# Performance work log

Hardware: AMD Instinct MI355X
Metric: run time of the kernel (lower is better)

## Reference

```python
import jax, jax.numpy as jnp
import numpy as np
import math

T = 4096
HID = 2048
H = 16
D = 128
RD = 64            # rotary_dim = head_dim * partial_rotary_factor (0.5)
THETA = 10000.0
EPS = 1e-6
GROUPS = 8
LAYER_IDX = 2
N_LAYERS = 32


def build_slope_tensor(num_heads):
    def get_slopes_power_of_2(n):
        start = 2 ** (-(2 ** (-(math.log2(n) - 3))))
        ratio = start
        return [start * ratio ** i for i in range(n)]
    if math.log2(num_heads).is_integer():
        return get_slopes_power_of_2(num_heads)
    closest = 2 ** math.floor(math.log2(num_heads))
    return (get_slopes_power_of_2(closest)
            + build_slope_tensor(2 * closest)[0::2][: num_heads - closest])


def compute_slope():
    base = np.array(build_slope_tensor(H), dtype=np.float32)
    return jnp.asarray(-base * (1 - (LAYER_IDX - 1) / (N_LAYERS - 1) + 1e-5), dtype=jnp.float32)


def setup_inputs() -> dict:
    key = jax.random.key(0)
    ks = jax.random.split(key, 8)
    s = 0.02
    return {
        "positions": jnp.arange(T, dtype=jnp.int32),
        "hidden_states": jax.random.normal(ks[0], (T, HID), dtype=jnp.float32),
        "recurrent_state": jnp.zeros((1, H, D, D), dtype=jnp.float32),
        "w_qkv": jax.random.normal(ks[1], (HID, 3 * H * D), dtype=jnp.float32) * s,
        "w_g": jax.random.normal(ks[2], (HID, H * D), dtype=jnp.float32) * s,
        "w_dense": jax.random.normal(ks[3], (H * D, HID), dtype=jnp.float32) * s,
        "q_norm_w": jnp.ones((D,), dtype=jnp.float32),
        "k_norm_w": jnp.ones((D,), dtype=jnp.float32),
        "g_norm_w": jnp.ones((H * D,), dtype=jnp.float32),
    }


def _rms(x, w):
    var = jnp.mean(jnp.square(x), axis=-1, keepdims=True)
    return x * jax.lax.rsqrt(var + EPS) * w


def _rope(x, positions):
    # partial neox-style rotary on first RD dims of each head
    inv_freq = 1.0 / (THETA ** (jnp.arange(0, RD, 2, dtype=jnp.float32) / RD))
    freqs = positions.astype(jnp.float32)[:, None] * inv_freq   # [T, RD/2]
    cos = jnp.cos(freqs)[:, None, :]                            # [T, 1, RD/2]
    sin = jnp.sin(freqs)[:, None, :]
    x1 = x[..., : RD // 2]
    x2 = x[..., RD // 2 : RD]
    x_pass = x[..., RD:]
    return jnp.concatenate([x1 * cos - x2 * sin, x2 * cos + x1 * sin, x_pass], axis=-1)


def reference(positions, hidden_states, recurrent_state,
              w_qkv, w_g, w_dense, q_norm_w, k_norm_w, g_norm_w):
    t = hidden_states.shape[0]
    qkv = (hidden_states @ w_qkv).reshape(t, 3, H, D)
    q, k, v = qkv[:, 0], qkv[:, 1], qkv[:, 2]
    q = _rms(q, q_norm_w)
    k = _rms(k, k_norm_w)
    q = _rope(q, positions)
    k = _rope(k, positions)

    slope = compute_slope()                    # [H], negative
    decay = jnp.exp(slope)                     # per-head per-step decay
    scale = D ** -0.5
    q = (q * scale).astype(jnp.float32)
    k = k.astype(jnp.float32)
    v = v.astype(jnp.float32)

    def step(S, qkv_t):
        q_t, k_t, v_t = qkv_t                  # each [H, D]
        S = S * decay[:, None, None] + k_t[:, :, None] * v_t[:, None, :]
        o_t = jnp.einsum('hk,hkv->hv', q_t, S)
        return S, o_t

    S0 = recurrent_state[0].astype(jnp.float32)   # [H, K, V]
    S_final, o = jax.lax.scan(step, S0, (q, k, v))
    attn = o.reshape(t, H * D)

    gate = jax.nn.sigmoid(hidden_states @ w_g)
    # GroupRMSNorm: normalize per group of size (H*D)/GROUPS, scale by full weight
    g = attn.reshape(t, GROUPS, (H * D) // GROUPS)
    var = jnp.mean(jnp.square(g), axis=-1, keepdims=True)
    g = (g * jax.lax.rsqrt(var + EPS)).reshape(t, H * D) * g_norm_w

    out = (g * gate) @ w_dense
    return out, S_final[None]
```

## Files before the change

kernel.cpp:

```cpp
#include <hip/hip_runtime.h>
#include <hip/hip_bf16.h>

using bf16x8 = __attribute__((ext_vector_type(8))) __bf16;
using f32x4  = __attribute__((ext_vector_type(4))) float;

constexpr int T_SEQ = 4096;
constexpr int HID_C = 2048;
constexpr int NH    = 16;
constexpr int QKV_N = 6144;

__device__ __forceinline__ float head_slope(int h) {
    return -exp2f(-0.5f * (float)(h + 1)) * 0.967751935483871f;
}

__device__ __forceinline__ ushort f2bfu(float f) {
    __hip_bfloat16 h = __float2bfloat16(f);
    return *(ushort*)&h;
}
__device__ __forceinline__ float bfu2f(ushort u) {
    union { unsigned int i; float f; } x; x.i = ((unsigned int)u) << 16; return x.f;
}

__device__ __forceinline__ void async16(const ushort* g, ushort* l) {
    __builtin_amdgcn_global_load_lds((const __attribute__((address_space(1))) void*)g,
                                     (__attribute__((address_space(3))) void*)l, 16, 0, 0);
}

template<int N> __device__ __forceinline__ void waitcnt_vm() {
    if constexpr (N == 0)      asm volatile("s_waitcnt vmcnt(0)" ::: "memory");
    else if constexpr (N == 2) asm volatile("s_waitcnt vmcnt(2)" ::: "memory");
    else if constexpr (N == 4) asm volatile("s_waitcnt vmcnt(4)" ::: "memory");
    else if constexpr (N == 6) asm volatile("s_waitcnt vmcnt(6)" ::: "memory");
}

__global__ __launch_bounds__(256) void cvt_bf16(const float* __restrict__ src,
                                                ushort* __restrict__ dst, int n) {
    int i = (blockIdx.x * 256 + threadIdx.x) * 8;
    if (i >= n) return;
    float4 a = *(const float4*)(src + i);
    float4 b = *(const float4*)(src + i + 4);
    ushort4 ua = {f2bfu(a.x), f2bfu(a.y), f2bfu(a.z), f2bfu(a.w)};
    ushort4 ub = {f2bfu(b.x), f2bfu(b.y), f2bfu(b.z), f2bfu(b.w)};
    *(ushort4*)(dst + i) = ua;
    *(ushort4*)(dst + i + 4) = ub;
}

__global__ __launch_bounds__(256) void transpose_cvt(const float* __restrict__ src,
                                                     ushort* __restrict__ dst,
                                                     int R, int C) {
    __shared__ ushort tile[64][68];
    int t = threadIdx.x;
    int tr = blockIdx.y * 64, tc = blockIdx.x * 64;
    int r0 = t >> 4;
    int c4 = (t & 15) << 2;
#pragma unroll
    for (int p = 0; p < 4; ++p) {
        int row = r0 + p * 16;
        float4 v = *(const float4*)&src[(size_t)(tr + row) * C + tc + c4];
        tile[row][c4 + 0] = f2bfu(v.x);
        tile[row][c4 + 1] = f2bfu(v.y);
        tile[row][c4 + 2] = f2bfu(v.z);
        tile[row][c4 + 3] = f2bfu(v.w);
    }
    __syncthreads();
#pragma unroll
    for (int p = 0; p < 4; ++p) {
        int orow = r0 + p * 16;
        ushort4 u;
        u.x = tile[c4 + 0][orow];
        u.y = tile[c4 + 1][orow];
        u.z = tile[c4 + 2][orow];
        u.w = tile[c4 + 3][orow];
        *(ushort4*)&dst[(size_t)(tc + orow) * R + tr + c4] = u;
    }
}

template<int MI, int BN>
__device__ __forceinline__ void gemm8_core(const ushort* __restrict__ Ag,
                                           const ushort* __restrict__ Bg,
                                           int K, int bm, int bn,
                                           ushort* sh, f32x4 (&acc)[MI][4]) {
    constexpr int WM = 16 / MI;
    constexpr int WN = 8 / WM;
    constexpr int MP = MI / 4;
    constexpr int SB = BN / 128;

    const int tid  = threadIdx.x;
    const int lane = tid & 63;
    const int wave = tid >> 6;
    const int lane15 = lane & 15, quad = lane >> 4;
    const int wm = wave / WN, wn = wave % WN;
    const int swz = lane15 & 7;

    ushort* const ldsA0 = sh;
    ushort* const ldsA1 = sh + 16384;
    ushort* const ldsB0 = sh + 32768;
    ushort* const ldsB1 = sh + 32768 + BN * 64;

    const int srow = lane >> 3;
    const int scol = ((lane & 7) ^ srow) << 3;
    const ushort* gA = Ag + (size_t)(bm + srow) * K + scol;
    const ushort* gB = Bg + (size_t)(bn + srow) * K + scol;
    const int ro  = wave * 16;
    const int roB = wave * 8 * SB;
    const int NT = K >> 6;

#define ST_A(L, h, k0) do { \
    _Pragma("unroll") for (int q = 0; q < 2; ++q) \
        async16(gA + (size_t)((h) * 128 + ro + q * 8) * K + (k0), (L) + ((h) * 128 + ro + q * 8) * 64); } while (0)
#define ST_B(L, h, k0) do { \
    _Pragma("unroll") for (int q = 0; q < SB; ++q) \
        async16(gB + (size_t)((h) * (BN / 2) + roB + q * 8) * K + (k0), (L) + ((h) * (BN / 2) + roB + q * 8) * 64); } while (0)
#define RD_A(L, p) do { \
    _Pragma("unroll") for (int m2 = 0; m2 < MP; ++m2) \
    _Pragma("unroll") for (int ks = 0; ks < 2; ++ks) \
        afr[m2][ks] = *(const bf16x8*)&(L)[(wm * (MI * 16) + ((p) * MP + m2) * 16 + lane15) * 64 + (((ks * 4 + quad) ^ swz) << 3)]; } while (0)
#define RD_B(L) do { \
    _Pragma("unroll") for (int j = 0; j < 4; ++j) \
    _Pragma("unroll") for (int ks = 0; ks < 2; ++ks) \
        bfr[j][ks] = *(const bf16x8*)&(L)[(wn * 64 + j * 16 + lane15) * 64 + (((ks * 4 + quad) ^ swz) << 3)]; } while (0)
#define MFMA_PH(p) do { \
    asm volatile("s_barrier" ::: "memory"); \
    asm volatile("s_waitcnt lgkmcnt(0)" ::: "memory"); \
    __builtin_amdgcn_s_setprio(1); \
    _Pragma("unroll") for (int m2 = 0; m2 < MP; ++m2) \
    _Pragma("unroll") for (int j = 0; j < 4; ++j) \
    _Pragma("unroll") for (int ks = 0; ks < 2; ++ks) \
        acc[(p) * MP + m2][j] = __builtin_amdgcn_mfma_f32_16x16x32_bf16(afr[m2][ks], bfr[j][ks], acc[(p) * MP + m2][j], 0, 0, 0); \
    __builtin_amdgcn_s_setprio(0); } while (0)
#define KTILE(LAc, LBc, LAn, LBn, t) do { \
    const int k0 = (t) << 6; \
    bf16x8 bfr[4][2]; \
    bf16x8 afr[MP][2]; \
    RD_B(LBc); RD_A(LAc, 0); \
    if ((t) + 1 < NT) ST_A(LAn, 0, k0 + 64); \
    MFMA_PH(0); \
    asm volatile("s_barrier" ::: "memory"); \
    RD_A(LAc, 1); \
    if ((t) + 1 < NT) ST_A(LAn, 1, k0 + 64); \
    MFMA_PH(1); \
    asm volatile("s_barrier" ::: "memory"); \
    RD_A(LAc, 2); \
    if ((t) + 2 < NT) ST_B(LBc, 0, k0 + 128); \
    MFMA_PH(2); \
    asm volatile("s_barrier" ::: "memory"); \
    RD_A(LAc, 3); \
    if ((t) + 2 < NT) ST_B(LBc, 1, k0 + 128); \
    MFMA_PH(3); \
    if ((t) + 2 < NT) { waitcnt_vm<2 * SB>(); } \
    else              { waitcnt_vm<0>(); } \
    asm volatile("s_barrier" ::: "memory"); } while (0)

    ST_A(ldsA0, 0, 0); ST_A(ldsA0, 1, 0);
    ST_B(ldsB0, 0, 0); ST_B(ldsB0, 1, 0);
    ST_B(ldsB1, 0, 64); ST_B(ldsB1, 1, 64);
    waitcnt_vm<2 * SB>();
    asm volatile("s_barrier" ::: "memory");

    for (int t = 0; t < NT; t += 2) {
        KTILE(ldsA0, ldsB0, ldsA1, ldsB1, t);
        KTILE(ldsA1, ldsB1, ldsA0, ldsB0, t + 1);
    }
#undef ST_A
#undef ST_B
#undef RD_A
#undef RD_B
#undef MFMA_PH
#undef KTILE
}

__global__ __launch_bounds__(512, 2) void gemm_fused(const ushort* __restrict__ A,
                                                     const ushort* __restrict__ Bcat,
                                                     ushort* __restrict__ qkv,
                                                     ushort* __restrict__ gate, int K) {
    __shared__ ushort sh[65536];
    int bid = blockIdx.x;
    int x = bid & 7, w = bid >> 3;
    int rm = x >> 2, rn = x & 3;
    int wm_i = w >> 3, wn_i = w & 7;
    int bm = (rm * 8 + wm_i) * 256;
    int bn = (rn * 8 + wn_i) * 256;
    f32x4 acc[8][4] = {};
    gemm8_core<8, 256>(A, Bcat, K, bm, bn, sh, acc);

    int lane = threadIdx.x & 63, wave = threadIdx.x >> 6;
    int lane15 = lane & 15, quad = lane >> 4;
    int wm = wave >> 2, wn = wave & 3;
    bool isg = bn >= QKV_N;
    ushort* outp = isg ? gate : qkv;
    int ncol = isg ? HID_C : QKV_N;
    int cb = (isg ? bn - QKV_N : bn) + wn * 64;
    int rb = bm + wm * 128;
#pragma unroll
    for (int i = 0; i < 8; ++i)
#pragma unroll
        for (int j = 0; j < 4; ++j) {
            int col = cb + j * 16 + lane15;
#pragma unroll
            for (int r = 0; r < 4; ++r) {
                float v = acc[i][j][r];
                if (isg) v = 1.0f / (1.0f + __expf(-v));
                outp[(size_t)(rb + i * 16 + quad * 4 + r) * ncol + col] = f2bfu(v);
            }
        }
}

__global__ __launch_bounds__(512, 2) void gemm_dense(const ushort* __restrict__ A,
                                                     const ushort* __restrict__ Bt,
                                                     float* __restrict__ Cout, int N, int K) {
    __shared__ ushort sh[49152];
    int bid = blockIdx.x;
    int x = bid & 7, w = bid >> 3;
    int rm = x >> 1, rn = x & 1;
    int wm_i = w >> 3, wn_i = w & 7;
    int bm = (rm * 4 + wm_i) * 256;
    int bn = (rn * 8 + wn_i) * 128;
    f32x4 acc[4][4] = {};
    gemm8_core<4, 128>(A, Bt, K, bm, bn, sh, acc);

    int lane = threadIdx.x & 63, wave = threadIdx.x >> 6;
    int lane15 = lane & 15, quad = lane >> 4;
    int wm = wave >> 1, wn = wave & 1;
    int cb = bn + wn * 64;
    int rb = bm + wm * 64;
#pragma unroll
    for (int i = 0; i < 4; ++i)
#pragma unroll
        for (int j = 0; j < 4; ++j) {
            int col = cb + j * 16 + lane15;
#pragma unroll
            for (int r = 0; r < 4; ++r)
                Cout[(size_t)(rb + i * 16 + quad * 4 + r) * N + col] = acc[i][j][r];
        }
}

__global__ __launch_bounds__(256) void rope_tab(const int* __restrict__ positions,
                                                float2* __restrict__ tab) {
    int i = blockIdx.x * 256 + threadIdx.x;
    int t = i >> 5, fi = i & 31;
    float inv = expf((float)fi * -0.2878231366f);
    float freq = (float)positions[t] * inv;
    float sn, cs;
    sincosf(freq, &sn, &cs);
    tab[i] = make_float2(cs, sn);
}

__global__ __launch_bounds__(256) void qk_rope_T(ushort* __restrict__ qkv,
                                                 const float2* __restrict__ tab,
                                                 const float* __restrict__ qw,
                                                 const float* __restrict__ kw,
                                                 ushort* __restrict__ kT,
                                                 ushort* __restrict__ vT) {
    __shared__ ushort tile[64][132];
    int bt = blockIdx.x;
    int kind = blockIdx.y >> 4, h = blockIdx.y & 15;
    int tid = threadIdx.x;
    int row = tid >> 2, c = tid & 3, d0 = c * 32;
    int t = bt * 64 + row;
    ushort* base = qkv + (size_t)t * QKV_N + kind * 2048 + h * 128 + d0;
    bf16x8 pk[4];
#pragma unroll
    for (int p = 0; p < 4; ++p) pk[p] = *(const bf16x8*)(base + p * 8);
    if (kind < 2) {
        float x[32];
        float ss = 0.f;
#pragma unroll
        for (int p = 0; p < 4; ++p)
#pragma unroll
            for (int i = 0; i < 8; ++i) {
                x[p * 8 + i] = (float)pk[p][i];
                ss += x[p * 8 + i] * x[p * 8 + i];
            }
        ss += __shfl_xor(ss, 1);
        ss += __shfl_xor(ss, 2);
        float rr = rsqrtf(ss * (1.0f / 128.0f) + 1e-6f);
        const float* w = (kind == 0) ? qw : kw;
#pragma unroll
        for (int i = 0; i < 32; ++i) x[i] *= rr * w[d0 + i];
#pragma unroll
        for (int i = 0; i < 32; ++i) {
            float p = __shfl_xor(x[i], 1);
            if (c < 2) {
                float2 rt = tab[t * 32 + i];
                x[i] = (c == 0) ? (x[i] * rt.x - p * rt.y) : (x[i] * rt.x + p * rt.y);
            }
        }
        float sc = (kind == 0) ? 0.08838834764831845f : 1.0f;
#pragma unroll
        for (int p = 0; p < 4; ++p)
#pragma unroll
            for (int i = 0; i < 8; ++i) pk[p][i] = (__bf16)(x[p * 8 + i] * sc);
#pragma unroll
        for (int p = 0; p < 4; ++p) *(bf16x8*)(base + p * 8) = pk[p];
    }
    if (kind >= 1) {
#pragma unroll
        for (int p = 0; p < 4; ++p) {
            ushort4* s = (ushort4*)&pk[p];
            *(ushort4*)&tile[row][d0 + p * 8]     = s[0];
            *(ushort4*)&tile[row][d0 + p * 8 + 4] = s[1];
        }
        __syncthreads();
        ushort* outT = ((kind == 1) ? kT : vT) + (size_t)(h * 128) * T_SEQ + bt * 64;
        int d = tid >> 1, half = tid & 1;
#pragma unroll
        for (int tt = 0; tt < 8; ++tt) {
            int tl = half * 32 + tt * 4;
            ushort4 u;
            u.x = tile[tl + 0][d];
            u.y = tile[tl + 1][d];
            u.z = tile[tl + 2][d];
            u.w = tile[tl + 3][d];
            *(ushort4*)&outT[(size_t)d * T_SEQ + tl] = u;
        }
    }
}

__global__ __launch_bounds__(256) void chunk_partial(const ushort* __restrict__ kT,
                                                     const ushort* __restrict__ vT,
                                                     float* __restrict__ PT) {
    int c = blockIdx.x, h = blockIdx.y;
    float slope = head_slope(h);
    float lam_inv = __expf(-slope);
    int tid = threadIdx.x, lane = tid & 63, wave = tid >> 6;
    int lane15 = lane & 15, quad = lane >> 4;
    int wv = (wave & 1) * 64, wd = (wave >> 1) * 64;
    const ushort* vbase = vT + (size_t)h * 128 * T_SEQ + c * 128;
    const ushort* kbase = kT + (size_t)h * 128 * T_SEQ + c * 128;
    f32x4 acc[4][4] = {};
#pragma unroll
    for (int j0 = 0; j0 < 128; j0 += 32) {
        float w8[8];
        w8[0] = __expf(slope * (float)(127 - (j0 + quad * 8)));
#pragma unroll
        for (int kk = 1; kk < 8; ++kk) w8[kk] = w8[kk - 1] * lam_inv;
        bf16x8 afr[4], bfr[4];
#pragma unroll
        for (int i = 0; i < 4; ++i) {
            bf16x8 v = *(const bf16x8*)&vbase[(size_t)(wv + i * 16 + lane15) * T_SEQ + j0 + quad * 8];
#pragma unroll
            for (int kk = 0; kk < 8; ++kk) afr[i][kk] = (__bf16)((float)v[kk] * w8[kk]);
        }
#pragma unroll
        for (int j = 0; j < 4; ++j)
            bfr[j] = *(const bf16x8*)&kbase[(size_t)(wd + j * 16 + lane15) * T_SEQ + j0 + quad * 8];
#pragma unroll
        for (int i = 0; i < 4; ++i)
#pragma unroll
            for (int j = 0; j < 4; ++j)
                acc[i][j] = __builtin_amdgcn_mfma_f32_16x16x32_bf16(afr[i], bfr[j], acc[i][j], 0, 0, 0);
    }
    float* out = PT + ((size_t)c * 16 + h) * 16384;
#pragma unroll
    for (int i = 0; i < 4; ++i)
#pragma unroll
        for (int j = 0; j < 4; ++j)
#pragma unroll
            for (int r = 0; r < 4; ++r)
                out[(size_t)(wv + i * 16 + quad * 4 + r) * 128 + wd + j * 16 + lane15] = acc[i][j][r];
}

__global__ __launch_bounds__(128) void scan_states(const float* __restrict__ PT,
                                                   const float* __restrict__ S0,
                                                   ushort* __restrict__ Spb,
                                                   float* __restrict__ Sfin) {
    int hv = blockIdx.x;
    int d = threadIdx.x;
    int h = hv >> 7, v = hv & 127;
    float lamC = __expf(head_slope(h) * 128.0f);
    float s = S0[(size_t)h * 16384 + d * 128 + v];
#pragma unroll
    for (int c = 0; c < 32; ++c) {
        size_t idx = ((size_t)c * 2048 + hv) * 128 + d;
        Spb[idx] = f2bfu(s);
        s = s * lamC + PT[idx];
    }
    Sfin[(size_t)h * 16384 + d * 128 + v] = s;
}

__global__ __launch_bounds__(256) void chunk_out(const ushort* __restrict__ qkv,
                                                 const ushort* __restrict__ vT,
                                                 const ushort* __restrict__ Spb,
                                                 ushort* __restrict__ o) {
    int c = blockIdx.x, h = blockIdx.y;
    float slope = head_slope(h);
    __shared__ ushort Ps[128 * 136];
    int tid = threadIdx.x, lane = tid & 63, wave = tid >> 6;
    int lane15 = lane & 15, quad = lane >> 4;
    int t0 = c * 128;
    int tt0 = wave, tt1 = 7 - wave;
    const ushort* qbase = qkv + (size_t)t0 * QKV_N + h * 128;
    const ushort* kbase = qbase + 2048;

    bf16x8 qf0[4], qf1[4];
#pragma unroll
    for (int ds = 0; ds < 4; ++ds) {
        qf0[ds] = *(const bf16x8*)&qbase[(size_t)(tt0 * 16 + lane15) * QKV_N + ds * 32 + quad * 8];
        qf1[ds] = *(const bf16x8*)&qbase[(size_t)(tt1 * 16 + lane15) * QKV_N + ds * 32 + quad * 8];
    }
    f32x4 s0a[4] = {};
    f32x4 s1a[8] = {};
#pragma unroll
    for (int st = 0; st < 8; ++st) {
        if (st <= tt1) {
            bf16x8 kf[4];
#pragma unroll
            for (int ds = 0; ds < 4; ++ds)
                kf[ds] = *(const bf16x8*)&kbase[(size_t)(st * 16 + lane15) * QKV_N + ds * 32 + quad * 8];
#pragma unroll
            for (int ds = 0; ds < 4; ++ds)
                s1a[st] = __builtin_amdgcn_mfma_f32_16x16x32_bf16(qf1[ds], kf[ds], s1a[st], 0, 0, 0);
            if (st <= tt0) {
#pragma unroll
                for (int ds = 0; ds < 4; ++ds)
                    s0a[st] = __builtin_amdgcn_mfma_f32_16x16x32_bf16(qf0[ds], kf[ds], s0a[st], 0, 0, 0);
            }
        }
    }
    int stmax0 = tt0 + ((tt0 & 1) ? 0 : 1);
    int stmax1 = tt1 + ((tt1 & 1) ? 0 : 1);
#pragma unroll
    for (int st = 0; st < 8; ++st) {
        if (st <= stmax1) {
#pragma unroll
            for (int r = 0; r < 4; ++r) {
                int t = tt1 * 16 + quad * 4 + r;
                int s = st * 16 + lane15;
                float val = 0.f;
                if (st <= tt1) val = (s <= t) ? s1a[st][r] * __expf(slope * (float)(t - s)) : 0.f;
                Ps[t * 136 + s] = f2bfu(val);
            }
        }
    }
#pragma unroll
    for (int st = 0; st < 5; ++st) {
        if (st <= stmax0) {
#pragma unroll
            for (int r = 0; r < 4; ++r) {
                int t = tt0 * 16 + quad * 4 + r;
                int s = st * 16 + lane15;
                float val = 0.f;
                if (st <= tt0) val = (s <= t) ? s0a[st][r] * __expf(slope * (float)(t - s)) : 0.f;
                Ps[t * 136 + s] = f2bfu(val);
            }
        }
    }
    __syncthreads();
    f32x4 oa0[8] = {};
    f32x4 oa1[8] = {};
    float lam0 = __expf(slope * (float)(tt0 * 16 + lane15 + 1));
    float lam1 = __expf(slope * (float)(tt1 * 16 + lane15 + 1));
    bf16x8 qs0[4], qs1[4];
#pragma unroll
    for (int ds = 0; ds < 4; ++ds)
#pragma unroll
        for (int kk = 0; kk < 8; ++kk) {
            qs0[ds][kk] = (__bf16)((float)qf0[ds][kk] * lam0);
            qs1[ds][kk] = (__bf16)((float)qf1[ds][kk] * lam1);
        }
    const ushort* spb = Spb + ((size_t)c * 2048 + h * 128) * 128;
#pragma unroll
    for (int vt = 0; vt < 8; ++vt)
#pragma unroll
        for (int ds = 0; ds < 4; ++ds) {
            bf16x8 bfrag = *(const bf16x8*)&spb[(vt * 16 + lane15) * 128 + ds * 32 + quad * 8];
            oa0[vt] = __builtin_amdgcn_mfma_f32_16x16x32_bf16(qs0[ds], bfrag, oa0[vt], 0, 0, 0);
            oa1[vt] = __builtin_amdgcn_mfma_f32_16x16x32_bf16(qs1[ds], bfrag, oa1[vt], 0, 0, 0);
        }
    const ushort* vbase = vT + (size_t)h * 128 * T_SEQ + t0;
    int ns0 = (tt0 + 2) >> 1, ns1 = (tt1 + 2) >> 1;
#pragma unroll
    for (int s32 = 0; s32 < 4; ++s32) {
        if (s32 < ns1) {
            bf16x8 af = *(const bf16x8*)&Ps[(tt1 * 16 + lane15) * 136 + s32 * 32 + quad * 8];
#pragma unroll
            for (int vt = 0; vt < 8; ++vt) {
                bf16x8 bfrag = *(const bf16x8*)&vbase[(size_t)(vt * 16 + lane15) * T_SEQ + s32 * 32 + quad * 8];
                oa1[vt] = __builtin_amdgcn_mfma_f32_16x16x32_bf16(af, bfrag, oa1[vt], 0, 0, 0);
            }
        }
    }
#pragma unroll
    for (int s32 = 0; s32 < 2; ++s32) {
        if (s32 < ns0) {
            bf16x8 af = *(const bf16x8*)&Ps[(tt0 * 16 + lane15) * 136 + s32 * 32 + quad * 8];
#pragma unroll
            for (int vt = 0; vt < 8; ++vt) {
                bf16x8 bfrag = *(const bf16x8*)&vbase[(size_t)(vt * 16 + lane15) * T_SEQ + s32 * 32 + quad * 8];
                oa0[vt] = __builtin_amdgcn_mfma_f32_16x16x32_bf16(af, bfrag, oa0[vt], 0, 0, 0);
            }
        }
    }
#pragma unroll
    for (int vt = 0; vt < 8; ++vt)
#pragma unroll
        for (int r = 0; r < 4; ++r) {
            o[(size_t)(t0 + tt0 * 16 + quad * 4 + r) * 2048 + h * 128 + vt * 16 + lane15] = f2bfu(oa0[vt][r]);
            o[(size_t)(t0 + tt1 * 16 + quad * 4 + r) * 2048 + h * 128 + vt * 16 + lane15] = f2bfu(oa1[vt][r]);
        }
}

__global__ __launch_bounds__(256) void gnorm_gate(const ushort* __restrict__ o,
                                                  const ushort* __restrict__ gate,
                                                  const float* __restrict__ gw,
                                                  ushort* __restrict__ gg) {
    int t = blockIdx.x;
    int tid = threadIdx.x;
    const ushort* op = o + (size_t)t * 2048 + tid * 8;
    bf16x8 xv = *(const bf16x8*)op;
    float x[8];
    float ss = 0.0f;
#pragma unroll
    for (int i = 0; i < 8; ++i) { x[i] = (float)xv[i]; ss += x[i] * x[i]; }
#pragma unroll
    for (int off = 16; off > 0; off >>= 1) ss += __shfl_xor(ss, off);
    float r = rsqrtf(ss * (1.0f / 256.0f) + 1e-6f);
    const ushort* gp = gate + (size_t)t * 2048;
#pragma unroll
    for (int i = 0; i < 8; ++i) {
        int j = tid * 8 + i;
        float val = x[i] * r * gw[j] * bfu2f(gp[j]);
        gg[(size_t)t * 2048 + j] = f2bfu(val);
    }
}

extern "C" void kernel_launch(void* const* d_in, const int* in_sizes, int n_in,
                              void* d_out, int out_size, void* d_ws, size_t ws_size,
                              hipStream_t stream) {
    const int* positions   = (const int*)d_in[0];
    const float* hidden    = (const float*)d_in[1];
    const float* S0        = (const float*)d_in[2];
    const float* w_qkv     = (const float*)d_in[3];
    const float* w_g       = (const float*)d_in[4];
    const float* w_dense   = (const float*)d_in[5];
    const float* qw        = (const float*)d_in[6];
    const float* kw        = (const float*)d_in[7];
    const float* gw        = (const float*)d_in[8];

    char* ws = (char*)d_ws;
    ushort* qkv     = (ushort*)ws;
    ushort* wqkv_t  = (ushort*)(ws + 50331648);
    ushort* wg_t    = (ushort*)(ws + 75497472);
    float2* ropet   = (float2*)(ws + 50331648);
    float*  PT      = (float*)(ws + 50331648);
    ushort* wd_t    = (ushort*)(ws + 83886080);
    ushort* gatebuf = (ushort*)(ws + 92274688);
    ushort* hid_b   = (ushort*)(ws + 109051904);
    ushort* Spb     = (ushort*)(ws + 109051904);
    ushort* kT      = (ushort*)(ws + 125829120);
    ushort* vT      = (ushort*)(ws + 142606336);
    ushort* gg      = (ushort*)ws;

    float* out  = (float*)d_out;
    float* Sfin = out + (size_t)T_SEQ * HID_C;
    ushort* obuf = (ushort*)d_out;

    cvt_bf16<<<T_SEQ * HID_C / (256 * 8), 256, 0, stream>>>(hidden, hid_b, T_SEQ * HID_C);
    transpose_cvt<<<dim3(QKV_N / 64, HID_C / 64), 256, 0, stream>>>(w_qkv, wqkv_t, HID_C, QKV_N);
    transpose_cvt<<<dim3(HID_C / 64, HID_C / 64), 256, 0, stream>>>(w_g, wg_t, HID_C, HID_C);
    transpose_cvt<<<dim3(HID_C / 64, HID_C / 64), 256, 0, stream>>>(w_dense, wd_t, HID_C, HID_C);

    gemm_fused<<<dim3(512), 512, 0, stream>>>(hid_b, wqkv_t, qkv, gatebuf, HID_C);

    rope_tab<<<T_SEQ * 32 / 256, 256, 0, stream>>>(positions, ropet);
    qk_rope_T<<<dim3(T_SEQ / 64, 48), 256, 0, stream>>>(qkv, ropet, qw, kw, kT, vT);

    chunk_partial<<<dim3(32, 16), 256, 0, stream>>>(kT, vT, PT);
    scan_states<<<2048, 128, 0, stream>>>(PT, S0, Spb, Sfin);
    chunk_out<<<dim3(32, 16), 256, 0, stream>>>(qkv, vT, Spb, obuf);
    gnorm_gate<<<T_SEQ, 256, 0, stream>>>(obuf, gatebuf, gw, gg);

    gemm_dense<<<dim3(256), 512, 0, stream>>>(gg, wd_t, out, HID_C, HID_C);
}
```

Before: 446.5 us.

## Simplify GEMM mainloop to single-barrier double-buffered K tiles

Replaces the four-phase, barrier-heavy K-tile schedule (staggered A/B prefetch with B prefetched two tiles ahead) with a plain double-buffered loop. Each iteration issues the next tile's A and B loads right after reading fragments, runs the MFMAs in two halves, then waits for all loads and takes one barrier. This removes several intra-tile barriers and lgkm waits. In exchange it loses the deeper B prefetch, and the full vmcnt(0) wait each tile may expose global load latency.

After: 443.2 us. About the same (-0.7%).

```diff
diff --git a/kernel.cpp b/kernel.cpp
--- a/kernel.cpp
+++ b/kernel.cpp
@@ -82,8 +82,9 @@
                                            ushort* sh, f32x4 (&acc)[MI][4]) {
     constexpr int WM = 16 / MI;
     constexpr int WN = 8 / WM;
-    constexpr int MP = MI / 4;
     constexpr int SB = BN / 128;
+    constexpr int AH = (MI >= 8) ? 2 : 1;
+    constexpr int MH = MI / AH;
 
     const int tid  = threadIdx.x;
     const int lane = tid & 63;
@@ -105,68 +106,72 @@
     const int roB = wave * 8 * SB;
     const int NT = K >> 6;
 
-#define ST_A(L, h, k0) do { \
+#define STAGE_A(L, k0) do { \
+    _Pragma("unroll") for (int h = 0; h < 2; ++h) \
     _Pragma("unroll") for (int q = 0; q < 2; ++q) \
         async16(gA + (size_t)((h) * 128 + ro + q * 8) * K + (k0), (L) + ((h) * 128 + ro + q * 8) * 64); } while (0)
-#define ST_B(L, h, k0) do { \
+#define STAGE_B(L, k0) do { \
+    _Pragma("unroll") for (int h = 0; h < 2; ++h) \
     _Pragma("unroll") for (int q = 0; q < SB; ++q) \
         async16(gB + (size_t)((h) * (BN / 2) + roB + q * 8) * K + (k0), (L) + ((h) * (BN / 2) + roB + q * 8) * 64); } while (0)
-#define RD_A(L, p) do { \
-    _Pragma("unroll") for (int m2 = 0; m2 < MP; ++m2) \
-    _Pragma("unroll") for (int ks = 0; ks < 2; ++ks) \
-        afr[m2][ks] = *(const bf16x8*)&(L)[(wm * (MI * 16) + ((p) * MP + m2) * 16 + lane15) * 64 + (((ks * 4 + quad) ^ swz) << 3)]; } while (0)
-#define RD_B(L) do { \
-    _Pragma("unroll") for (int j = 0; j < 4; ++j) \
-    _Pragma("unroll") for (int ks = 0; ks < 2; ++ks) \
-        bfr[j][ks] = *(const bf16x8*)&(L)[(wn * 64 + j * 16 + lane15) * 64 + (((ks * 4 + quad) ^ swz) << 3)]; } while (0)
-#define MFMA_PH(p) do { \
-    asm volatile("s_barrier" ::: "memory"); \
-    asm volatile("s_waitcnt lgkmcnt(0)" ::: "memory"); \
-    __builtin_amdgcn_s_setprio(1); \
-    _Pragma("unroll") for (int m2 = 0; m2 < MP; ++m2) \
-    _Pragma("unroll") for (int j = 0; j < 4; ++j) \
-    _Pragma("unroll") for (int ks = 0; ks < 2; ++ks) \
-        acc[(p) * MP + m2][j] = __builtin_amdgcn_mfma_f32_16x16x32_bf16(afr[m2][ks], bfr[j][ks], acc[(p) * MP + m2][j], 0, 0, 0); \
-    __builtin_amdgcn_s_setprio(0); } while (0)
-#define KTILE(LAc, LBc, LAn, LBn, t) do { \
-    const int k0 = (t) << 6; \
-    bf16x8 bfr[4][2]; \
-    bf16x8 afr[MP][2]; \
-    RD_B(LBc); RD_A(LAc, 0); \
-    if ((t) + 1 < NT) ST_A(LAn, 0, k0 + 64); \
-    MFMA_PH(0); \
-    asm volatile("s_barrier" ::: "memory"); \
-    RD_A(LAc, 1); \
-    if ((t) + 1 < NT) ST_A(LAn, 1, k0 + 64); \
-    MFMA_PH(1); \
-    asm volatile("s_barrier" ::: "memory"); \
-    RD_A(LAc, 2); \
-    if ((t) + 2 < NT) ST_B(LBc, 0, k0 + 128); \
-    MFMA_PH(2); \
-    asm volatile("s_barrier" ::: "memory"); \
-    RD_A(LAc, 3); \
-    if ((t) + 2 < NT) ST_B(LBc, 1, k0 + 128); \
-    MFMA_PH(3); \
-    if ((t) + 2 < NT) { waitcnt_vm<2 * SB>(); } \
-    else              { waitcnt_vm<0>(); } \
-    asm volatile("s_barrier" ::: "memory"); } while (0)
-
-    ST_A(ldsA0, 0, 0); ST_A(ldsA0, 1, 0);
-    ST_B(ldsB0, 0, 0); ST_B(ldsB0, 1, 0);
-    ST_B(ldsB1, 0, 64); ST_B(ldsB1, 1, 64);
-    waitcnt_vm<2 * SB>();
+
+    STAGE_A(ldsA0, 0);
+    STAGE_B(ldsB0, 0);
+    waitcnt_vm<0>();
     asm volatile("s_barrier" ::: "memory");
 
-    for (int t = 0; t < NT; t += 2) {
-        KTILE(ldsA0, ldsB0, ldsA1, ldsB1, t);
-        KTILE(ldsA1, ldsB1, ldsA0, ldsB0, t + 1);
-    }
-#undef ST_A
-#undef ST_B
-#undef RD_A
-#undef RD_B
-#undef MFMA_PH
-#undef KTILE
+    for (int t = 0; t < NT; ++t) {
+        const ushort* LA = (t & 1) ? ldsA1 : ldsA0;
+        const ushort* LB = (t & 1) ? ldsB1 : ldsB0;
+        ushort* LAn = (t & 1) ? ldsA0 : ldsA1;
+        ushort* LBn = (t & 1) ? ldsB0 : ldsB1;
+        bf16x8 bfr[4][2];
+#pragma unroll
+        for (int j = 0; j < 4; ++j)
+#pragma unroll
+            for (int ks = 0; ks < 2; ++ks)
+                bfr[j][ks] = *(const bf16x8*)&LB[(wn * 64 + j * 16 + lane15) * 64 + (((ks * 4 + quad) ^ swz) << 3)];
+        bf16x8 af0[MH][2];
+#pragma unroll
+        for (int i = 0; i < MH; ++i)
+#pragma unroll
+            for (int ks = 0; ks < 2; ++ks)
+                af0[i][ks] = *(const bf16x8*)&LA[(wm * (MI * 16) + i * 16 + lane15) * 64 + (((ks * 4 + quad) ^ swz) << 3)];
+        if (t + 1 < NT) {
+            STAGE_A(LAn, (t + 1) << 6);
+            STAGE_B(LBn, (t + 1) << 6);
+        }
+        __builtin_amdgcn_s_setprio(1);
+#pragma unroll
+        for (int i = 0; i < MH; ++i)
+#pragma unroll
+            for (int j = 0; j < 4; ++j)
+#pragma unroll
+                for (int ks = 0; ks < 2; ++ks)
+                    acc[i][j] = __builtin_amdgcn_mfma_f32_16x16x32_bf16(af0[i][ks], bfr[j][ks], acc[i][j], 0, 0, 0);
+        __builtin_amdgcn_s_setprio(0);
+        if constexpr (AH == 2) {
+            bf16x8 af1[MH][2];
+#pragma unroll
+            for (int i = 0; i < MH; ++i)
+#pragma unroll
+                for (int ks = 0; ks < 2; ++ks)
+                    af1[i][ks] = *(const bf16x8*)&LA[(wm * (MI * 16) + (MH + i) * 16 + lane15) * 64 + (((ks * 4 + quad) ^ swz) << 3)];
+            __builtin_amdgcn_s_setprio(1);
+#pragma unroll
+            for (int i = 0; i < MH; ++i)
+#pragma unroll
+                for (int j = 0; j < 4; ++j)
+#pragma unroll
+                    for (int ks = 0; ks < 2; ++ks)
+                        acc[MH + i][j] = __builtin_amdgcn_mfma_f32_16x16x32_bf16(af1[i][ks], bfr[j][ks], acc[MH + i][j], 0, 0, 0);
+            __builtin_amdgcn_s_setprio(0);
+        }
+        waitcnt_vm<0>();
+        asm volatile("s_barrier" ::: "memory");
+    }
+#undef STAGE_A
+#undef STAGE_B
 }
 
 __global__ __launch_bounds__(512, 2) void gemm_fused(const ushort* __restrict__ A,
```
